# Kernel tuning notes

Hardware: AMD Instinct MI355X
Metric: run time of the kernel (lower is better)

Reference implementation:

```python
import jax, jax.numpy as jnp
import numpy as np

EMBED = 1024
HEADS = 16

def setup_inputs() -> dict:
    key = jax.random.key(0)
    ks = jax.random.split(key, 6)
    N, S = 1, 4096
    half = EMBED // 2
    x = jax.random.normal(ks[0], (N, S, EMBED), dtype=jnp.float32)
    Wq = jax.random.normal(ks[1], (half, half), dtype=jnp.float32) * 0.02
    Wk = jax.random.normal(ks[2], (half, half), dtype=jnp.float32) * 0.02
    Wv = jax.random.normal(ks[3], (half, half), dtype=jnp.float32) * 0.02
    Wo = jax.random.normal(ks[4], (EMBED, half), dtype=jnp.float32) * 0.02
    bo = jnp.zeros((EMBED,), dtype=jnp.float32)
    return {"x": x, "Wq": Wq, "Wk": Wk, "Wv": Wv, "Wo": Wo, "bo": bo}

def reference(x, Wq, Wk, Wv, Wo, bo):
    N, S, E = x.shape
    H = HEADS
    Dh = (E // 2) // H                 # per-head dim of the half-width projections (32)
    scale = float(E // H) ** 0.5       # original scales by head_dim = embed/heads = 64
    left = x[..., : E // 2]            # only the left chunk feeds attention in the source
    # torch Linear: y = x @ W.T (no bias)
    q = (left @ Wq.T).reshape(N, S, H, Dh)
    k = (left @ Wk.T).reshape(N, S, H, Dh)
    v = (left @ Wv.T).reshape(N, S, H, Dh)
    energy = jnp.einsum('nqhd,nkhd->nqkh', q, k)          # [N,S,S,H] full score tensor
    att = jax.nn.softmax(energy / scale, axis=2)          # softmax over key axis
    out = jnp.einsum('nqkh,nkhd->nqhd', att, v)           # [N,S,H,Dh]
    out = out.reshape(N, S, E // 2)
    return out @ Wo.T + bo                                # fc_out: half -> embed
```

## Files before the change

### kernel.cpp

```cpp
#include <hip/hip_runtime.h>
#include <stdint.h>


#define SEQ    4096
#define DMODEL 1024
#define DHALF  512
#define NH     16
#define DH     32

typedef __attribute__((ext_vector_type(4))) float facc4;
typedef __attribute__((ext_vector_type(8))) short bfrag8;

#define MFMA_BF16(a, b, c) __builtin_amdgcn_mfma_f32_16x16x32_bf16((a), (b), (c), 0, 0, 0)

static __device__ __forceinline__ void gll16(const void* g, void* l) {
    typedef const __attribute__((address_space(1))) void GV;
    typedef __attribute__((address_space(3))) void LV;
    __builtin_amdgcn_global_load_lds((GV*)g, (LV*)l, 16, 0, 0);
}

static __device__ __forceinline__ uint16_t f2b(float x) {
    uint32_t u = __float_as_uint(x);
    return (uint16_t)((u + 0x7FFFu + ((u >> 16) & 1u)) >> 16);
}
static __device__ __forceinline__ float b2f(uint16_t b) {
    return __uint_as_float(((uint32_t)b) << 16);
}

static __device__ __forceinline__ bfrag8 cvt8perm(float4 a, float4 b) {
    uint32_t u0 = __float_as_uint(a.x) + 0x8000u, u1 = __float_as_uint(a.y) + 0x8000u;
    uint32_t u2 = __float_as_uint(a.z) + 0x8000u, u3 = __float_as_uint(a.w) + 0x8000u;
    uint32_t u4 = __float_as_uint(b.x) + 0x8000u, u5 = __float_as_uint(b.y) + 0x8000u;
    uint32_t u6 = __float_as_uint(b.z) + 0x8000u, u7 = __float_as_uint(b.w) + 0x8000u;
    union { uint32_t w[4]; bfrag8 r; } u;
    u.w[0] = __builtin_amdgcn_perm(u1, u0, 0x07060302u);
    u.w[1] = __builtin_amdgcn_perm(u3, u2, 0x07060302u);
    u.w[2] = __builtin_amdgcn_perm(u5, u4, 0x07060302u);
    u.w[3] = __builtin_amdgcn_perm(u7, u6, 0x07060302u);
    return u.r;
}

__global__ __launch_bounds__(256) void convert_w(
    const float* __restrict__ Wq, const float* __restrict__ Wk,
    const float* __restrict__ Wv, const float* __restrict__ Wo,
    const float* __restrict__ x,
    uint16_t* __restrict__ q, uint16_t* __restrict__ k,
    uint16_t* __restrict__ v, uint16_t* __restrict__ o,
    uint16_t* __restrict__ xb)
{
    int zz = blockIdx.x;
    if (zz >= 640) {
        size_t g = (size_t)(zz - 640) * 2048 + (size_t)threadIdx.x * 8;
        int row = (int)(g >> 9);
        int col = (int)(g & 511);
        const float* src = &x[(size_t)row * DMODEL + col];
        float4 a = *(const float4*)src;
        float4 b = *(const float4*)(src + 4);
        *(bfrag8*)&xb[g] = cvt8perm(a, b);
        return;
    }
    const float* src; uint16_t* dst; size_t off;
    if      (zz < 128) { src = Wq; dst = q; off = (size_t)zz * 2048; }
    else if (zz < 256) { src = Wk; dst = k; off = (size_t)(zz - 128) * 2048; }
    else if (zz < 384) { src = Wv; dst = v; off = (size_t)(zz - 256) * 2048; }
    else               { src = Wo; dst = o; off = (size_t)(zz - 384) * 2048; }
    size_t i = off + (size_t)threadIdx.x * 8;
    float4 a = *(const float4*)&src[i];
    float4 b = *(const float4*)&src[i + 4];
    *(bfrag8*)&dst[i] = cvt8perm(a, b);
}

__device__ __forceinline__ void gemm128(
    const uint16_t* __restrict__ A, int lda,
    const uint16_t* __restrict__ B, int ldb,
    void* __restrict__ C, int ldc, int cF32,
    const float* __restrict__ bias, float scale,
    int Kd, int m0, int n0)
{
    __shared__ __align__(16) uint16_t As[2][128 * 64];
    __shared__ __align__(16) uint16_t Bs[2][128 * 64];

    const int tid  = threadIdx.x;
    const int lane = tid & 63;
    const int wv   = tid >> 6;
    const int lo   = lane & 15;
    const int quad = lane >> 4;
    const int rb   = (wv >> 1) * 64;
    const int cb   = (wv & 1) * 64;

    const facc4 ZACC = {0.f, 0.f, 0.f, 0.f};
    facc4 acc[4][4];
#pragma unroll
    for (int i = 0; i < 4; ++i)
#pragma unroll
        for (int j = 0; j < 4; ++j) acc[i][j] = ZACC;

    const int lrow8 = lane >> 3;
    const int scol  = (((lane & 7) ^ lrow8) << 3);
    const uint16_t* gA[4];
    const uint16_t* gB[4];
#pragma unroll
    for (int ii = 0; ii < 4; ++ii) {
        gA[ii] = &A[(size_t)(m0 + wv * 32 + ii * 8 + lrow8) * lda + scol];
        gB[ii] = &B[(size_t)(n0 + wv * 32 + ii * 8 + lrow8) * ldb + scol];
    }
    const int dd[4] = { wv * 2048, wv * 2048 + 512, wv * 2048 + 1024, wv * 2048 + 1536 };

    const int rdo0 = lo * 64 + (((quad) ^ (lo & 7)) << 3);
    const int rdo1 = lo * 64 + (((4 + quad) ^ (lo & 7)) << 3);

#pragma unroll
    for (int ii = 0; ii < 4; ++ii) {
        gll16(gA[ii], &As[0][dd[ii]]);
        gll16(gB[ii], &Bs[0][dd[ii]]);
    }
    __syncthreads();

    int p = 0;
    for (int kt = 0; kt < Kd; kt += 64) {
        const bool more = (kt + 64 < Kd);
        if (more) {
#pragma unroll
            for (int ii = 0; ii < 4; ++ii) {
                gll16(gA[ii] + kt + 64, &As[1 - p][dd[ii]]);
                gll16(gB[ii] + kt + 64, &Bs[1 - p][dd[ii]]);
            }
        }

        {
            bfrag8 af[4], bf[4];
#pragma unroll
            for (int i = 0; i < 4; ++i) {
                af[i] = *(const bfrag8*)&As[p][rb * 64 + i * 1024 + rdo0];
                bf[i] = *(const bfrag8*)&Bs[p][cb * 64 + i * 1024 + rdo0];
            }
#pragma unroll
            for (int i = 0; i < 4; ++i)
#pragma unroll
                for (int j = 0; j < 4; ++j)
                    acc[i][j] = MFMA_BF16(bf[j], af[i], acc[i][j]);
        }
        {
            bfrag8 af[4], bf[4];
#pragma unroll
            for (int i = 0; i < 4; ++i) {
                af[i] = *(const bfrag8*)&As[p][rb * 64 + i * 1024 + rdo1];
                bf[i] = *(const bfrag8*)&Bs[p][cb * 64 + i * 1024 + rdo1];
            }
#pragma unroll
            for (int i = 0; i < 4; ++i)
#pragma unroll
                for (int j = 0; j < 4; ++j)
                    acc[i][j] = MFMA_BF16(bf[j], af[i], acc[i][j]);
        }

        if (more) {
            __syncthreads();
            p ^= 1;
        }
    }

#pragma unroll
    for (int i = 0; i < 4; ++i) {
        const size_t row = (size_t)(m0 + rb + i * 16 + lo);
#pragma unroll
        for (int j = 0; j < 4; ++j) {
            const int colb = n0 + cb + j * 16 + quad * 4;
            float4 bv = {0.f, 0.f, 0.f, 0.f};
            if (bias) bv = *(const float4*)&bias[colb];
            float v0 = acc[i][j][0] * scale + bv.x;
            float v1 = acc[i][j][1] * scale + bv.y;
            float v2 = acc[i][j][2] * scale + bv.z;
            float v3 = acc[i][j][3] * scale + bv.w;
            if (cF32) {
                float4 o = {v0, v1, v2, v3};
                *(float4*)&((float*)C)[row * ldc + colb] = o;
            } else {
                uint2 o;
                o.x = (uint32_t)f2b(v0) | ((uint32_t)f2b(v1) << 16);
                o.y = (uint32_t)f2b(v2) | ((uint32_t)f2b(v3) << 16);
                *(uint2*)&((uint16_t*)C)[row * ldc + colb] = o;
            }
        }
    }
}

#define SC_Q (0.125f * 1.4426950408889634f)

__global__ __launch_bounds__(256, 2) void qkv_kernel(
    const uint16_t* __restrict__ xb,
    const uint16_t* __restrict__ Wqb, const uint16_t* __restrict__ Wkb,
    const uint16_t* __restrict__ Wvb,
    uint16_t* __restrict__ Q, uint16_t* __restrict__ K, uint16_t* __restrict__ V)
{
    const int z = blockIdx.z;
    const uint16_t* W = (z == 0) ? Wqb : (z == 1) ? Wkb : Wvb;
    uint16_t* Out     = (z == 0) ? Q   : (z == 1) ? K   : V;
    float scale       = (z == 0) ? SC_Q : 1.0f;
    gemm128(xb, DHALF, W, DHALF, Out, DHALF, 0, nullptr, scale, DHALF,
            blockIdx.y * 128, blockIdx.x * 128);
}

__global__ __launch_bounds__(256, 2) void outproj_kernel(
    const uint16_t* __restrict__ O, const uint16_t* __restrict__ Wob,
    const float* __restrict__ bo, float* __restrict__ Y)
{
    gemm128(O, DHALF, Wob, DHALF, Y, DMODEL, 1, bo, 1.0f, DHALF,
            blockIdx.y * 128, blockIdx.x * 128);
}

__global__ __launch_bounds__(512) void attn_kernel(
    const uint16_t* __restrict__ Q, const uint16_t* __restrict__ Kb,
    const uint16_t* __restrict__ Vb, uint16_t* __restrict__ Op,
    float* __restrict__ lbuf, int kspan)
{
    __shared__ __align__(16) uint16_t Ks[2][128 * 40];
    __shared__ __align__(16) uint16_t Vt[2][32 * 128];

    const int tid  = threadIdx.x;
    const int lane = tid & 63;
    const int wv   = tid >> 6;
    const int lo   = lane & 15;
    const int quad = lane >> 4;

    const int f  = blockIdx.x + 16 * blockIdx.y + 256 * blockIdx.z;
    const int pp = (f & 7) | ((f >> 7) << 3);
    const int h  = pp & 15;
    const int sp = pp >> 4;
    const int q0 = ((f >> 3) & 15) * 256;

    const int srow = tid >> 2;
    const int skq  = (tid & 3) * 8;

    const facc4 ZACC = {0.f, 0.f, 0.f, 0.f};

    bfrag8 qf[2];
    qf[0] = *(const bfrag8*)&Q[(size_t)(q0 + wv * 32 + lo) * DHALF + h * DH + quad * 8];
    qf[1] = *(const bfrag8*)&Q[(size_t)(q0 + wv * 32 + 16 + lo) * DHALF + h * DH + quad * 8];

    bfrag8 ones;
#pragma unroll
    for (int j = 0; j < 8; ++j) ones[j] = (short)0x3F80;

    int vt_w[8];
    {
        int pb = ((srow >> 5) << 2) | ((srow >> 2) & 3);
        int pw = (((srow >> 4) & 1) << 2) | (srow & 3);
#pragma unroll
        for (int j = 0; j < 8; ++j) {
            int d  = skq + j;
            int Rd = ((d & 7) + 2 * (d >> 3)) & 7;
            vt_w[j] = d * 128 + (((pb + Rd) & 15) << 3) + pw;
        }
    }
    int vt_r[4][2];
#pragma unroll
    for (int dt = 0; dt < 2; ++dt) {
        int d  = dt * 16 + lo;
        int Rd = ((d & 7) + 2 * (d >> 3)) & 7;
#pragma unroll
        for (int c = 0; c < 4; ++c)
            vt_r[c][dt] = d * 128 + ((((c * 4 + quad) + Rd) & 15) << 3);
    }
    const int ks_r = lo * 40 + quad * 8;

    const uint16_t* kp = &Kb[(size_t)(sp * kspan + srow) * DHALF + h * DH + skq];
    const uint16_t* vp = &Vb[(size_t)(sp * kspan + srow) * DHALF + h * DH + skq];

    facc4 oacc[2][2], oaccL[2];
    oacc[0][0] = ZACC; oacc[0][1] = ZACC;
    oacc[1][0] = ZACC; oacc[1][1] = ZACC;
    oaccL[0] = ZACC; oaccL[1] = ZACC;

    float4 kreg = *(const float4*)kp;
    float4 vreg = *(const float4*)vp;
    kp += 128 * DHALF;
    vp += 128 * DHALF;

#define STAGE(BUF) do {                                                       \
        *(float4*)&Ks[BUF][srow * 40 + skq] = kreg;                           \
        const uint16_t* vsp = (const uint16_t*)&vreg;                         \
        _Pragma("unroll")                                                     \
        for (int j = 0; j < 8; ++j) Vt[BUF][vt_w[j]] = vsp[j];                \
    } while (0)

#define HALF(BUF, HH) do {                                                    \
        uint2 w0[4], w1[4];                                                   \
        _Pragma("unroll")                                                     \
        for (int t4 = 0; t4 < 4; ++t4) {                                      \
            bfrag8 kf = *(const bfrag8*)&Ks[BUF][(4 * HH + t4) * 640 + ks_r]; \
            facc4 s0 = MFMA_BF16(kf, qf[0], ZACC);                            \
            facc4 s1 = MFMA_BF16(kf, qf[1], ZACC);                            \
            uint32_t a0 = __float_as_uint(__builtin_amdgcn_exp2f(s0[0])) + 0x8000u; \
            uint32_t a1 = __float_as_uint(__builtin_amdgcn_exp2f(s0[1])) + 0x8000u; \
            uint32_t a2 = __float_as_uint(__builtin_amdgcn_exp2f(s0[2])) + 0x8000u; \
            uint32_t a3 = __float_as_uint(__builtin_amdgcn_exp2f(s0[3])) + 0x8000u; \
            w0[t4].x = __builtin_amdgcn_perm(a1, a0, 0x07060302u);            \
            w0[t4].y = __builtin_amdgcn_perm(a3, a2, 0x07060302u);            \
            uint32_t b0 = __float_as_uint(__builtin_amdgcn_exp2f(s1[0])) + 0x8000u; \
            uint32_t b1 = __float_as_uint(__builtin_amdgcn_exp2f(s1[1])) + 0x8000u; \
            uint32_t b2 = __float_as_uint(__builtin_amdgcn_exp2f(s1[2])) + 0x8000u; \
            uint32_t b3 = __float_as_uint(__builtin_amdgcn_exp2f(s1[3])) + 0x8000u; \
            w1[t4].x = __builtin_amdgcn_perm(b1, b0, 0x07060302u);            \
            w1[t4].y = __builtin_amdgcn_perm(b3, b2, 0x07060302u);            \
        }                                                                     \
        union PU { uint2 u2[2]; bfrag8 f; } pu;                               \
        bfrag8 pf0[2], pf1[2];                                                \
        pu.u2[0] = w0[0]; pu.u2[1] = w0[1]; pf0[0] = pu.f;                    \
        pu.u2[0] = w0[2]; pu.u2[1] = w0[3]; pf0[1] = pu.f;                    \
        pu.u2[0] = w1[0]; pu.u2[1] = w1[1]; pf1[0] = pu.f;                    \
        pu.u2[0] = w1[2]; pu.u2[1] = w1[3]; pf1[1] = pu.f;                    \
        _Pragma("unroll")                                                     \
        for (int cc = 0; cc < 2; ++cc) {                                      \
            _Pragma("unroll")                                                 \
            for (int dt = 0; dt < 2; ++dt) {                                  \
                bfrag8 vf = *(const bfrag8*)&Vt[BUF][vt_r[2 * HH + cc][dt]];  \
                oacc[0][dt] = MFMA_BF16(pf0[cc], vf, oacc[0][dt]);            \
                oacc[1][dt] = MFMA_BF16(pf1[cc], vf, oacc[1][dt]);            \
            }                                                                 \
            oaccL[0] = MFMA_BF16(pf0[cc], ones, oaccL[0]);                    \
            oaccL[1] = MFMA_BF16(pf1[cc], ones, oaccL[1]);                    \
        }                                                                     \
    } while (0)

#define TILE(BUF) do { HALF(BUF, 0); HALF(BUF, 1); } while (0)

    STAGE(0);
    __syncthreads();

    const int nt = kspan >> 7;
    for (int t = 0; t < nt; t += 2) {
        kreg = *(const float4*)kp;
        vreg = *(const float4*)vp;
        kp += 128 * DHALF; vp += 128 * DHALF;
        TILE(0);
        STAGE(1);
        __syncthreads();

        const bool more = (t + 2 < nt);
        if (more) {
            kreg = *(const float4*)kp;
            vreg = *(const float4*)vp;
            kp += 128 * DHALF; vp += 128 * DHALF;
        }
        TILE(1);
        if (more) {
            STAGE(0);
            __syncthreads();
        }
    }
#undef STAGE
#undef HALF
#undef TILE

    if (lo == 0) {
#pragma unroll
        for (int g = 0; g < 2; ++g)
#pragma unroll
            for (int r = 0; r < 4; ++r)
                lbuf[((size_t)sp * NH + h) * SEQ + q0 + wv * 32 + g * 16 + quad * 4 + r] =
                    oaccL[g][r];
    }

    uint16_t* Od = Op + (size_t)sp * SEQ * DHALF;
#pragma unroll
    for (int g = 0; g < 2; ++g) {
#pragma unroll
        for (int r = 0; r < 4; ++r) {
            int row = q0 + wv * 32 + g * 16 + quad * 4 + r;
            Od[(size_t)row * DHALF + h * DH + lo]      = f2b(oacc[g][0][r]);
            Od[(size_t)row * DHALF + h * DH + 16 + lo] = f2b(oacc[g][1][r]);
        }
    }
}

__global__ __launch_bounds__(256) void combine_kernel(
    const uint16_t* __restrict__ Op, const float* __restrict__ lbuf,
    uint16_t* __restrict__ O, int ns)
{
    int t   = blockIdx.x * 256 + threadIdx.x;
    int row = t >> 6;
    int cb  = (t & 63) << 3;
    int h   = cb >> 5;
    float l = 0.f;
    float acc[8] = {0.f, 0.f, 0.f, 0.f, 0.f, 0.f, 0.f, 0.f};
    for (int sp = 0; sp < ns; ++sp) {
        l += lbuf[((size_t)sp * NH + h) * SEQ + row];
        bfrag8 a = *(const bfrag8*)&Op[(size_t)sp * SEQ * DHALF + (size_t)row * DHALF + cb];
#pragma unroll
        for (int j = 0; j < 8; ++j) acc[j] += b2f((uint16_t)a[j]);
    }
    float inv = 1.0f / l;
    bfrag8 o;
#pragma unroll
    for (int j = 0; j < 8; ++j) o[j] = (short)f2b(acc[j] * inv);
    *(bfrag8*)&O[(size_t)row * DHALF + cb] = o;
}

extern "C" void kernel_launch(void* const* d_in, const int* in_sizes, int n_in,
                              void* d_out, int out_size, void* d_ws, size_t ws_size,
                              hipStream_t stream)
{
    const float* x  = (const float*)d_in[0];
    const float* Wq = (const float*)d_in[1];
    const float* Wk = (const float*)d_in[2];
    const float* Wv = (const float*)d_in[3];
    const float* Wo = (const float*)d_in[4];
    const float* bo = (const float*)d_in[5];

    const int ns = 2;

    uint16_t* Wqb = (uint16_t*)d_ws;
    uint16_t* Wkb = Wqb + (size_t)DHALF * DHALF;
    uint16_t* Wvb = Wkb + (size_t)DHALF * DHALF;
    uint16_t* Wob = Wvb + (size_t)DHALF * DHALF;
    uint16_t* Q   = Wob + (size_t)DMODEL * DHALF;
    uint16_t* K   = Q + (size_t)SEQ * DHALF;
    uint16_t* V   = K + (size_t)SEQ * DHALF;
    uint16_t* O   = V + (size_t)SEQ * DHALF;
    uint16_t* Op  = O + (size_t)SEQ * DHALF;
    float*  lbuf  = (float*)(Op + (size_t)ns * SEQ * DHALF);
    uint16_t* xb  = O;

    convert_w<<<1664, 256, 0, stream>>>(Wq, Wk, Wv, Wo, x, Wqb, Wkb, Wvb, Wob, xb);
    qkv_kernel<<<dim3(DHALF / 128, SEQ / 128, 3), 256, 0, stream>>>(
        xb, Wqb, Wkb, Wvb, Q, K, V);
    attn_kernel<<<dim3(SEQ / 256, NH, ns), 512, 0, stream>>>(Q, K, V, Op, lbuf, SEQ / ns);
    combine_kernel<<<1024, 256, 0, stream>>>(Op, lbuf, O, ns);
    outproj_kernel<<<dim3(DMODEL / 128, SEQ / 128), 256, 0, stream>>>(
        O, Wob, bo, (float*)d_out);
}
```

Measured before the change: 160.0 us.

## Split key tile across wave halves in attention and reduce partials via LDS

Each attention block now covers 128 queries instead of 256, and its 8 waves form two groups of 4 that each process half of every 128-key tile. This doubles the grid to 1024 blocks for better occupancy and load balance across CUs. Each wave does half the MFMA work per staged tile. In exchange, the partial output and row-sum accumulators are reduced through shared memory at the end, which adds an extra sync and LDS traffic, and K/V tiles are loaded twice as often per query.

```diff
diff --git a/kernel.cpp b/kernel.cpp
--- a/kernel.cpp
+++ b/kernel.cpp
@@ -222,12 +222,14 @@
     const int wv   = tid >> 6;
     const int lo   = lane & 15;
     const int quad = lane >> 4;
-
-    const int f  = blockIdx.x + 16 * blockIdx.y + 256 * blockIdx.z;
-    const int pp = (f & 7) | ((f >> 7) << 3);
+    const int qg   = wv & 3;
+    const int kh   = wv >> 2;
+
+    const int f  = blockIdx.x + 32 * blockIdx.y + 512 * blockIdx.z;
+    const int pp = (f & 7) | ((f >> 8) << 3);
     const int h  = pp & 15;
     const int sp = pp >> 4;
-    const int q0 = ((f >> 3) & 15) * 256;
+    const int q0 = ((f >> 3) & 31) * 128;
 
     const int srow = tid >> 2;
     const int skq  = (tid & 3) * 8;
@@ -235,8 +237,8 @@
     const facc4 ZACC = {0.f, 0.f, 0.f, 0.f};
 
     bfrag8 qf[2];
-    qf[0] = *(const bfrag8*)&Q[(size_t)(q0 + wv * 32 + lo) * DHALF + h * DH + quad * 8];
-    qf[1] = *(const bfrag8*)&Q[(size_t)(q0 + wv * 32 + 16 + lo) * DHALF + h * DH + quad * 8];
+    qf[0] = *(const bfrag8*)&Q[(size_t)(q0 + qg * 32 + lo) * DHALF + h * DH + quad * 8];
+    qf[1] = *(const bfrag8*)&Q[(size_t)(q0 + qg * 32 + 16 + lo) * DHALF + h * DH + quad * 8];
 
     bfrag8 ones;
 #pragma unroll
@@ -253,16 +255,16 @@
             vt_w[j] = d * 128 + (((pb + Rd) & 15) << 3) + pw;
         }
     }
-    int vt_r[4][2];
+    int vt_r[2][2];
 #pragma unroll
     for (int dt = 0; dt < 2; ++dt) {
         int d  = dt * 16 + lo;
         int Rd = ((d & 7) + 2 * (d >> 3)) & 7;
 #pragma unroll
-        for (int c = 0; c < 4; ++c)
-            vt_r[c][dt] = d * 128 + ((((c * 4 + quad) + Rd) & 15) << 3);
-    }
-    const int ks_r = lo * 40 + quad * 8;
+        for (int cc = 0; cc < 2; ++cc)
+            vt_r[cc][dt] = d * 128 + (((((2 * kh + cc) * 4 + quad) + Rd) & 15) << 3);
+    }
+    const int ks_r = kh * 2560 + lo * 40 + quad * 8;
 
     const uint16_t* kp = &Kb[(size_t)(sp * kspan + srow) * DHALF + h * DH + skq];
     const uint16_t* vp = &Vb[(size_t)(sp * kspan + srow) * DHALF + h * DH + skq];
@@ -284,11 +286,11 @@
         for (int j = 0; j < 8; ++j) Vt[BUF][vt_w[j]] = vsp[j];                \
     } while (0)
 
-#define HALF(BUF, HH) do {                                                    \
+#define HALFK(BUF) do {                                                       \
         uint2 w0[4], w1[4];                                                   \
         _Pragma("unroll")                                                     \
         for (int t4 = 0; t4 < 4; ++t4) {                                      \
-            bfrag8 kf = *(const bfrag8*)&Ks[BUF][(4 * HH + t4) * 640 + ks_r]; \
+            bfrag8 kf = *(const bfrag8*)&Ks[BUF][t4 * 640 + ks_r];            \
             facc4 s0 = MFMA_BF16(kf, qf[0], ZACC);                            \
             facc4 s1 = MFMA_BF16(kf, qf[1], ZACC);                            \
             uint32_t a0 = __float_as_uint(__builtin_amdgcn_exp2f(s0[0])) + 0x8000u; \
@@ -314,7 +316,7 @@
         for (int cc = 0; cc < 2; ++cc) {                                      \
             _Pragma("unroll")                                                 \
             for (int dt = 0; dt < 2; ++dt) {                                  \
-                bfrag8 vf = *(const bfrag8*)&Vt[BUF][vt_r[2 * HH + cc][dt]];  \
+                bfrag8 vf = *(const bfrag8*)&Vt[BUF][vt_r[cc][dt]];           \
                 oacc[0][dt] = MFMA_BF16(pf0[cc], vf, oacc[0][dt]);            \
                 oacc[1][dt] = MFMA_BF16(pf1[cc], vf, oacc[1][dt]);            \
             }                                                                 \
@@ -323,8 +325,6 @@
         }                                                                     \
     } while (0)
 
-#define TILE(BUF) do { HALF(BUF, 0); HALF(BUF, 1); } while (0)
-
     STAGE(0);
     __syncthreads();
 
@@ -333,7 +333,7 @@
         kreg = *(const float4*)kp;
         vreg = *(const float4*)vp;
         kp += 128 * DHALF; vp += 128 * DHALF;
-        TILE(0);
+        HALFK(0);
         STAGE(1);
         __syncthreads();
 
@@ -343,22 +343,47 @@
             vreg = *(const float4*)vp;
             kp += 128 * DHALF; vp += 128 * DHALF;
         }
-        TILE(1);
+        HALFK(1);
         if (more) {
             STAGE(0);
             __syncthreads();
         }
     }
 #undef STAGE
-#undef HALF
-#undef TILE
+#undef HALFK
+
+    __syncthreads();
+    {
+        float* ob = (float*)&Ks[0][0];
+        float* lb = (float*)&Vt[0][0];
+        float* d  = ob + (size_t)(qg * 64 + lane) * 20;
+        float* dl = lb + (size_t)(qg * 64 + lane) * 12;
+        if (kh == 1) {
+            *(facc4*)(d + 0)  = oacc[0][0];
+            *(facc4*)(d + 4)  = oacc[0][1];
+            *(facc4*)(d + 8)  = oacc[1][0];
+            *(facc4*)(d + 12) = oacc[1][1];
+            *(facc4*)(dl + 0) = oaccL[0];
+            *(facc4*)(dl + 4) = oaccL[1];
+        }
+        __syncthreads();
+        if (kh == 0) {
+            oacc[0][0] += *(const facc4*)(d + 0);
+            oacc[0][1] += *(const facc4*)(d + 4);
+            oacc[1][0] += *(const facc4*)(d + 8);
+            oacc[1][1] += *(const facc4*)(d + 12);
+            oaccL[0]   += *(const facc4*)(dl + 0);
+            oaccL[1]   += *(const facc4*)(dl + 4);
+        }
+    }
+    if (kh != 0) return;
 
     if (lo == 0) {
 #pragma unroll
         for (int g = 0; g < 2; ++g)
 #pragma unroll
             for (int r = 0; r < 4; ++r)
-                lbuf[((size_t)sp * NH + h) * SEQ + q0 + wv * 32 + g * 16 + quad * 4 + r] =
+                lbuf[((size_t)sp * NH + h) * SEQ + q0 + qg * 32 + g * 16 + quad * 4 + r] =
                     oaccL[g][r];
     }
 
@@ -367,7 +392,7 @@
     for (int g = 0; g < 2; ++g) {
 #pragma unroll
         for (int r = 0; r < 4; ++r) {
-            int row = q0 + wv * 32 + g * 16 + quad * 4 + r;
+            int row = q0 + qg * 32 + g * 16 + quad * 4 + r;
             Od[(size_t)row * DHALF + h * DH + lo]      = f2b(oacc[g][0][r]);
             Od[(size_t)row * DHALF + h * DH + 16 + lo] = f2b(oacc[g][1][r]);
         }
@@ -425,7 +450,7 @@
     convert_w<<<1664, 256, 0, stream>>>(Wq, Wk, Wv, Wo, x, Wqb, Wkb, Wvb, Wob, xb);
     qkv_kernel<<<dim3(DHALF / 128, SEQ / 128, 3), 256, 0, stream>>>(
         xb, Wqb, Wkb, Wvb, Q, K, V);
-    attn_kernel<<<dim3(SEQ / 256, NH, ns), 512, 0, stream>>>(Q, K, V, Op, lbuf, SEQ / ns);
+    attn_kernel<<<dim3(SEQ / 128, NH, ns), 512, 0, stream>>>(Q, K, V, Op, lbuf, SEQ / ns);
     combine_kernel<<<1024, 256, 0, stream>>>(Op, lbuf, O, ns);
     outproj_kernel<<<dim3(DMODEL / 128, SEQ / 128), 256, 0, stream>>>(
         O, Wob, bo, (float*)d_out);
```

After: 165.8 us. +3.6%, slower.
